# Optimization experiments

Hardware: AMD Instinct MI355X
Metric: run time of the kernel (lower is better)

The kernel has to match this reference:

```python
import jax, jax.numpy as jnp
import numpy as np

D = 768
B = 32
N = 768


def setup_inputs() -> dict:
    key = jax.random.key(0)
    k1, k2, k3, k4 = jax.random.split(key, 4)
    stdv = 1.0 / np.sqrt(D)
    X = jax.random.normal(k1, (B, N, D), dtype=jnp.float32)
    adj = jax.random.uniform(k2, (B, N, N), dtype=jnp.float32)
    W_l = jax.random.uniform(k3, (D, D), dtype=jnp.float32, minval=-stdv, maxval=stdv)
    W_l1 = jax.random.uniform(k4, (D, D), dtype=jnp.float32, minval=-stdv, maxval=stdv)
    return {"X": X, "adj": adj, "W_l": W_l, "W_l1": W_l1}


def _row_normalize(adj):
    # rowsum^-1 with inf -> 0 (rows summing to zero stay zero)
    rowsum = adj.sum(axis=-1, keepdims=True)  # [B, N, 1]
    r_inv = jnp.where(rowsum == 0, 0.0, 1.0 / rowsum)
    return adj * r_inv


def reference(X, adj, W_l, W_l1):
    # X: [B, N, D], adj: [B, N, N]
    adj_n = _row_normalize(adj)
    e1 = jnp.einsum('bnd,de->bne', X, W_l1)        # message transform
    e11 = jnp.einsum('bnm,bmd->bnd', adj_n, e1)    # aggregate
    X1 = jnp.einsum('bnd,de->bne', X, W_l)         # self transform
    h = X1 + e11
    return jax.nn.leaky_relu(h, negative_slope=0.01)
```

## Files before the change

kernel.cpp:

```cpp
#include <hip/hip_runtime.h>
#include <hip/hip_bf16.h>
#include <cstdint>
#include <cstddef>

#define BN_ROWS 24576
#define DD 768
#define BE (768*768)
#define BM 384
#define BN_T 192
#define BK 64

typedef __attribute__((ext_vector_type(8))) short bf16x8;
typedef __attribute__((ext_vector_type(4))) float f32x4;

static __device__ __forceinline__ unsigned short f2bf(float f) {
  unsigned int u = __builtin_bit_cast(unsigned int, f);
  unsigned int lsb = (u >> 16) & 1u;
  u += 0x7fffu + lsb;
  return (unsigned short)(u >> 16);
}


__global__ __launch_bounds__(256) void convertX(const float* __restrict__ x,
                                                unsigned short* __restrict__ xb, int n4) {
  int idx = blockIdx.x * blockDim.x + threadIdx.x;
  int stride = gridDim.x * blockDim.x;
  for (int i = idx; i < n4; i += stride) {
    float4 v = reinterpret_cast<const float4*>(x)[i];
    ushort4 o;
    o.x = f2bf(v.x); o.y = f2bf(v.y); o.z = f2bf(v.z); o.w = f2bf(v.w);
    reinterpret_cast<ushort4*>(xb)[i] = o;
  }
}

__global__ __launch_bounds__(256) void convertWT(const float* __restrict__ Wl,
                                                 const float* __restrict__ Wl1,
                                                 unsigned short* __restrict__ WlT,
                                                 unsigned short* __restrict__ Wl1T) {
  int tid = blockIdx.x * blockDim.x + threadIdx.x;
  if (tid < BE) {
    int d = tid / DD, e = tid % DD;
    WlT[e * DD + d]  = f2bf(Wl[tid]);
    Wl1T[e * DD + d] = f2bf(Wl1[tid]);
  }
}

__global__ __launch_bounds__(256) void adjNorm(const float* __restrict__ adj,
                                               unsigned short* __restrict__ adjnb) {
  int wid = threadIdx.x >> 6, lane = threadIdx.x & 63;
  int row = blockIdx.x * 4 + wid;
  const float4* a = reinterpret_cast<const float4*>(adj + (size_t)row * DD);
  float4 v[3];
  float s = 0.f;
  #pragma unroll
  for (int i = 0; i < 3; ++i) {
    v[i] = a[i * 64 + lane];
    s += (v[i].x + v[i].y) + (v[i].z + v[i].w);
  }
  #pragma unroll
  for (int off = 32; off; off >>= 1) s += __shfl_down(s, off);
  s = __shfl(s, 0);
  float rinv = (s == 0.f) ? 0.f : 1.f / s;
  ushort4* o = reinterpret_cast<ushort4*>(adjnb + (size_t)row * DD);
  #pragma unroll
  for (int i = 0; i < 3; ++i) {
    ushort4 u;
    u.x = f2bf(v[i].x * rinv); u.y = f2bf(v[i].y * rinv);
    u.z = f2bf(v[i].z * rinv); u.w = f2bf(v[i].w * rinv);
    o[i * 64 + lane] = u;
  }
}


template<int MODE>
__global__ __launch_bounds__(512, 2) void gemm8(
    const unsigned short* __restrict__ P0,
    const unsigned short* __restrict__ P1,
    const unsigned short* __restrict__ P2,
    const unsigned short* __restrict__ P3,
    void* __restrict__ outp)
{
  __shared__ char smem[147456];
  constexpr int NT = MODE ? 24 : 12;
  const int tid = threadIdx.x, lane = tid & 63;
  const int wid = tid >> 6, wr = wid >> 1, wc = wid & 1;

  const int logical = (blockIdx.x & 7) * 32 + (blockIdx.x >> 3);

  const unsigned short *Ab0, *Bb0, *Ab1 = nullptr, *Bb1 = nullptr;
  int mt, nt, b;
  if (MODE == 0) {
    mt = logical >> 2; nt = logical & 3;
    b = mt >> 1;
    Ab0 = P0 + (size_t)mt * BM * DD;
    Bb0 = P1 + (size_t)nt * BN_T * DD;
  } else {
    b = logical >> 3; int r = logical & 7; mt = r >> 2; nt = r & 3;
    size_t bo = (size_t)b * BE;
    Ab0 = P0 + bo + (size_t)mt * BM * DD;
    Bb0 = P1 + bo + (size_t)nt * BN_T * DD;
    Ab1 = P2 + bo + (size_t)mt * BM * DD;
    Bb1 = P3 + (size_t)nt * BN_T * DD;
  }

  const int srow = tid >> 3;
  const int sslot = (tid & 7) ^ (srow & 7);
  const int lane_off = srow * DD + sslot * 8;
  const int wchunk = (tid >> 6) * 1024;

  auto stage = [&](int s, int g) {
    int sc = s < NT ? s : 0;
    const unsigned short* base;
    int kk;
    if (MODE == 1 && sc >= 12) { kk = sc - 12; base = (g == 2) ? Bb1 : Ab1; }
    else                       { kk = sc;      base = (g == 2) ? Bb0 : Ab0; }
    const unsigned short* p = base + (size_t)(g == 1 ? 192 : 0) * DD + kk * BK + lane_off;
    char* dst = smem + ((g == 2) ? (98304 + (s & 1) * 24576)
                                 : ((s & 1) * 49152 + g * 24576)) + wchunk;
    #pragma unroll
    for (int i = 0; i < 3; ++i) {
      __builtin_amdgcn_global_load_lds(
          (const __attribute__((address_space(1))) void*)(p + (size_t)i * 64 * DD),
          (__attribute__((address_space(3))) void*)(dst + i * 8192), 16, 0, 0);
    }
  };

  auto frag = [&](int bufbase, int rowbase, int ks) -> bf16x8 {
    int row = rowbase + (lane & 15);
    int slot = (ks * 4 + (lane >> 4)) ^ (row & 7);
    return *reinterpret_cast<const bf16x8*>(smem + bufbase + row * 128 + slot * 16);
  };

  f32x4 acc[6][6] = {};
  bf16x8 af[6], bf[6];

  stage(0, 0); stage(0, 1); stage(0, 2);
  asm volatile("s_waitcnt vmcnt(0)" ::: "memory");
  __builtin_amdgcn_s_barrier();

  for (int t = 0; t < NT; ++t) {
    const int Ab = (t & 1) * 49152;
    const int Bb = 98304 + (t & 1) * 24576;

    #pragma unroll
    for (int i = 0; i < 6; ++i) {
      af[i] = frag(Ab, wr * 96 + i * 16, 0);
      bf[i] = frag(Bb, wc * 96 + i * 16, 0);
    }
    stage(t + 1, 0); stage(t + 1, 1); stage(t + 1, 2);
    __builtin_amdgcn_s_barrier();
    __builtin_amdgcn_s_setprio(1);
    #pragma unroll
    for (int mi = 0; mi < 6; ++mi)
      #pragma unroll
      for (int ni = 0; ni < 6; ++ni)
        acc[mi][ni] = __builtin_amdgcn_mfma_f32_16x16x32_bf16(af[mi], bf[ni], acc[mi][ni], 0, 0, 0);
    __builtin_amdgcn_s_setprio(0);
    __builtin_amdgcn_s_barrier();

    #pragma unroll
    for (int i = 0; i < 6; ++i) {
      af[i] = frag(Ab, wr * 96 + i * 16, 1);
      bf[i] = frag(Bb, wc * 96 + i * 16, 1);
    }
    __builtin_amdgcn_s_barrier();
    __builtin_amdgcn_s_setprio(1);
    #pragma unroll
    for (int mi = 0; mi < 6; ++mi)
      #pragma unroll
      for (int ni = 0; ni < 6; ++ni)
        acc[mi][ni] = __builtin_amdgcn_mfma_f32_16x16x32_bf16(af[mi], bf[ni], acc[mi][ni], 0, 0, 0);
    __builtin_amdgcn_s_setprio(0);
    asm volatile("s_waitcnt vmcnt(0)" ::: "memory");
    __builtin_amdgcn_s_barrier();
  }

  if (MODE == 0) {
    unsigned short* ob = (unsigned short*)outp + (size_t)b * BE;
    const int mloc = (mt & 1) * BM + wr * 96 + (lane >> 4) * 4;
    #pragma unroll
    for (int mi = 0; mi < 6; ++mi)
      #pragma unroll
      for (int ni = 0; ni < 6; ++ni) {
        int m = mloc + mi * 16;
        int d = nt * BN_T + wc * 96 + ni * 16 + (lane & 15);
        f32x4 v = acc[mi][ni];
        ushort4 o;
        o.x = f2bf(v[0]); o.y = f2bf(v[1]); o.z = f2bf(v[2]); o.w = f2bf(v[3]);
        *reinterpret_cast<ushort4*>(ob + (size_t)d * DD + m) = o;
      }
  } else {
    float* ob = (float*)outp + (size_t)b * BE;
    const int mloc = mt * BM + wr * 96 + (lane >> 4) * 4;
    #pragma unroll
    for (int mi = 0; mi < 6; ++mi)
      #pragma unroll
      for (int ni = 0; ni < 6; ++ni) {
        int m = mloc + mi * 16;
        int n = nt * BN_T + wc * 96 + ni * 16 + (lane & 15);
        f32x4 v = acc[mi][ni];
        #pragma unroll
        for (int j = 0; j < 4; ++j) {
          float x = v[j];
          ob[(size_t)(m + j) * DD + n] = x > 0.f ? x : 0.01f * x;
        }
      }
  }
}


extern "C" void kernel_launch(void* const* d_in, const int* in_sizes, int n_in,
                              void* d_out, int out_size, void* d_ws, size_t ws_size,
                              hipStream_t stream) {
  const float* X   = (const float*)d_in[0];
  const float* adj = (const float*)d_in[1];
  const float* Wl  = (const float*)d_in[2];
  const float* Wl1 = (const float*)d_in[3];
  float* out = (float*)d_out;

  char* ws = (char*)d_ws;
  const size_t SZ = (size_t)BN_ROWS * DD * 2;
  unsigned short* Xb    = (unsigned short*)(ws);
  unsigned short* adjnb = (unsigned short*)(ws + SZ);
  unsigned short* e1T   = (unsigned short*)(ws + 2 * SZ);
  unsigned short* WlT   = (unsigned short*)(ws + 3 * SZ);
  unsigned short* Wl1T  = (unsigned short*)(ws + 3 * SZ + (size_t)BE * 2);

  convertX<<<4096, 256, 0, stream>>>(X, Xb, (BN_ROWS * DD) / 4);
  convertWT<<<(BE + 255) / 256, 256, 0, stream>>>(Wl, Wl1, WlT, Wl1T);
  adjNorm<<<BN_ROWS / 4, 256, 0, stream>>>(adj, adjnb);
  gemm8<0><<<256, 512, 0, stream>>>(Xb, Wl1T, nullptr, nullptr, e1T);
  gemm8<1><<<256, 512, 0, stream>>>(adjnb, e1T, Xb, WlT, out);
}
```

Before: 154.5 us.

## Triple-buffer GEMM with BK=32 and tile the weight transpose through LDS

The GEMM main loop moves from a double-buffered BK=64 scheme to a three-stage ring of BK=32 buffers. Loads are issued two stages ahead, partial vmcnt waits replace full drains, and each warp group loads either A or B with a new XOR swizzle. This aims to overlap global-to-LDS traffic with MFMA work and cut LDS use, at the cost of twice as many iterations and barriers. Separately, the weight transpose-convert now goes through a padded shared-memory tile so both reads and writes are coalesced.

```diff
diff --git a/kernel.cpp b/kernel.cpp
--- a/kernel.cpp
+++ b/kernel.cpp
@@ -8,7 +8,9 @@
 #define BE (768*768)
 #define BM 384
 #define BN_T 192
-#define BK 64
+#define BK 32
+#define ABUF 24576
+#define BUFSZ 36864
 
 typedef __attribute__((ext_vector_type(8))) short bf16x8;
 typedef __attribute__((ext_vector_type(4))) float f32x4;
@@ -37,11 +39,27 @@
                                                  const float* __restrict__ Wl1,
                                                  unsigned short* __restrict__ WlT,
                                                  unsigned short* __restrict__ Wl1T) {
-  int tid = blockIdx.x * blockDim.x + threadIdx.x;
-  if (tid < BE) {
-    int d = tid / DD, e = tid % DD;
-    WlT[e * DD + d]  = f2bf(Wl[tid]);
-    Wl1T[e * DD + d] = f2bf(Wl1[tid]);
+  __shared__ float tile[64][65];
+  int tr = blockIdx.x / 12, tc = blockIdx.x % 12;
+  int c = threadIdx.x & 63, r0 = threadIdx.x >> 6;
+  const float* srcs[2] = {Wl, Wl1};
+  unsigned short* dsts[2] = {WlT, Wl1T};
+  #pragma unroll
+  for (int m = 0; m < 2; ++m) {
+    const float* src = srcs[m];
+    #pragma unroll
+    for (int i = 0; i < 16; ++i) {
+      int r = r0 + i * 4;
+      tile[r][c] = src[(size_t)(tr * 64 + r) * DD + tc * 64 + c];
+    }
+    __syncthreads();
+    unsigned short* dst = dsts[m];
+    #pragma unroll
+    for (int i = 0; i < 16; ++i) {
+      int r2 = r0 + i * 4;
+      dst[(size_t)(tc * 64 + r2) * DD + tr * 64 + c] = f2bf(tile[c][r2]);
+    }
+    __syncthreads();
   }
 }
 
@@ -80,8 +98,8 @@
     const unsigned short* __restrict__ P3,
     void* __restrict__ outp)
 {
-  __shared__ char smem[147456];
-  constexpr int NT = MODE ? 24 : 12;
+  __shared__ char smem[3 * BUFSZ];
+  constexpr int NT = MODE ? 48 : 24;
   const int tid = threadIdx.x, lane = tid & 63;
   const int wid = tid >> 6, wr = wid >> 1, wc = wid & 1;
 
@@ -103,75 +121,72 @@
     Bb1 = P3 + (size_t)nt * BN_T * DD;
   }
 
-  const int srow = tid >> 3;
-  const int sslot = (tid & 7) ^ (srow & 7);
-  const int lane_off = srow * DD + sslot * 8;
-  const int wchunk = (tid >> 6) * 1024;
-
-  auto stage = [&](int s, int g) {
+  const int r_in = lane >> 2;
+  const int s_in = lane & 3;
+
+  auto stage = [&](int s) {
     int sc = s < NT ? s : 0;
-    const unsigned short* base;
+    const int buf = (s % 3) * BUFSZ;
+    const unsigned short *Abase, *Bbase;
     int kk;
-    if (MODE == 1 && sc >= 12) { kk = sc - 12; base = (g == 2) ? Bb1 : Ab1; }
-    else                       { kk = sc;      base = (g == 2) ? Bb0 : Ab0; }
-    const unsigned short* p = base + (size_t)(g == 1 ? 192 : 0) * DD + kk * BK + lane_off;
-    char* dst = smem + ((g == 2) ? (98304 + (s & 1) * 24576)
-                                 : ((s & 1) * 49152 + g * 24576)) + wchunk;
-    #pragma unroll
-    for (int i = 0; i < 3; ++i) {
-      __builtin_amdgcn_global_load_lds(
-          (const __attribute__((address_space(1))) void*)(p + (size_t)i * 64 * DD),
-          (__attribute__((address_space(3))) void*)(dst + i * 8192), 16, 0, 0);
+    if (MODE == 1 && sc >= 24) { kk = sc - 24; Abase = Ab1; Bbase = Bb1; }
+    else                       { kk = sc;      Abase = Ab0; Bbase = Bb0; }
+    if (wid < 4) {
+      #pragma unroll
+      for (int i = 0; i < 6; ++i) {
+        int row = wid * 96 + i * 16 + r_in;
+        int slot = s_in ^ ((row >> 1) & 3);
+        const unsigned short* src = Abase + (size_t)row * DD + kk * BK + slot * 8;
+        __builtin_amdgcn_global_load_lds(
+            (const __attribute__((address_space(1))) void*)src,
+            (__attribute__((address_space(3))) void*)(smem + buf + (wid * 96 + i * 16) * 64),
+            16, 0, 0);
+      }
+    } else {
+      #pragma unroll
+      for (int i = 0; i < 3; ++i) {
+        int row = (wid - 4) * 48 + i * 16 + r_in;
+        int slot = s_in ^ ((row >> 1) & 3);
+        const unsigned short* src = Bbase + (size_t)row * DD + kk * BK + slot * 8;
+        __builtin_amdgcn_global_load_lds(
+            (const __attribute__((address_space(1))) void*)src,
+            (__attribute__((address_space(3))) void*)(smem + buf + ABUF + ((wid - 4) * 48 + i * 16) * 64),
+            16, 0, 0);
+      }
     }
   };
 
-  auto frag = [&](int bufbase, int rowbase, int ks) -> bf16x8 {
-    int row = rowbase + (lane & 15);
-    int slot = (ks * 4 + (lane >> 4)) ^ (row & 7);
-    return *reinterpret_cast<const bf16x8*>(smem + bufbase + row * 128 + slot * 16);
+  const int ks = lane >> 4;
+  auto frag = [&](int off, int row) -> bf16x8 {
+    int slot = ks ^ ((row >> 1) & 3);
+    return *reinterpret_cast<const bf16x8*>(smem + off + row * 64 + slot * 16);
   };
 
   f32x4 acc[6][6] = {};
-  bf16x8 af[6], bf[6];
-
-  stage(0, 0); stage(0, 1); stage(0, 2);
-  asm volatile("s_waitcnt vmcnt(0)" ::: "memory");
-  __builtin_amdgcn_s_barrier();
+
+  stage(0); stage(1);
 
   for (int t = 0; t < NT; ++t) {
-    const int Ab = (t & 1) * 49152;
-    const int Bb = 98304 + (t & 1) * 24576;
-
+    stage(t + 2);
+    if (wid < 4) asm volatile("s_waitcnt vmcnt(12)" ::: "memory");
+    else         asm volatile("s_waitcnt vmcnt(6)"  ::: "memory");
+    __builtin_amdgcn_s_barrier();
+
+    const int bufA = (t % 3) * BUFSZ;
+    const int bufB = bufA + ABUF;
+    bf16x8 af[6], bg[6];
     #pragma unroll
     for (int i = 0; i < 6; ++i) {
-      af[i] = frag(Ab, wr * 96 + i * 16, 0);
-      bf[i] = frag(Bb, wc * 96 + i * 16, 0);
-    }
-    stage(t + 1, 0); stage(t + 1, 1); stage(t + 1, 2);
-    __builtin_amdgcn_s_barrier();
+      af[i] = frag(bufA, wr * 96 + i * 16 + (lane & 15));
+      bg[i] = frag(bufB, wc * 96 + i * 16 + (lane & 15));
+    }
     __builtin_amdgcn_s_setprio(1);
     #pragma unroll
     for (int mi = 0; mi < 6; ++mi)
       #pragma unroll
       for (int ni = 0; ni < 6; ++ni)
-        acc[mi][ni] = __builtin_amdgcn_mfma_f32_16x16x32_bf16(af[mi], bf[ni], acc[mi][ni], 0, 0, 0);
+        acc[mi][ni] = __builtin_amdgcn_mfma_f32_16x16x32_bf16(af[mi], bg[ni], acc[mi][ni], 0, 0, 0);
     __builtin_amdgcn_s_setprio(0);
-    __builtin_amdgcn_s_barrier();
-
-    #pragma unroll
-    for (int i = 0; i < 6; ++i) {
-      af[i] = frag(Ab, wr * 96 + i * 16, 1);
-      bf[i] = frag(Bb, wc * 96 + i * 16, 1);
-    }
-    __builtin_amdgcn_s_barrier();
-    __builtin_amdgcn_s_setprio(1);
-    #pragma unroll
-    for (int mi = 0; mi < 6; ++mi)
-      #pragma unroll
-      for (int ni = 0; ni < 6; ++ni)
-        acc[mi][ni] = __builtin_amdgcn_mfma_f32_16x16x32_bf16(af[mi], bf[ni], acc[mi][ni], 0, 0, 0);
-    __builtin_amdgcn_s_setprio(0);
-    asm volatile("s_waitcnt vmcnt(0)" ::: "memory");
     __builtin_amdgcn_s_barrier();
   }
 
@@ -227,7 +242,7 @@
   unsigned short* Wl1T  = (unsigned short*)(ws + 3 * SZ + (size_t)BE * 2);
 
   convertX<<<4096, 256, 0, stream>>>(X, Xb, (BN_ROWS * DD) / 4);
-  convertWT<<<(BE + 255) / 256, 256, 0, stream>>>(Wl, Wl1, WlT, Wl1T);
+  convertWT<<<144, 256, 0, stream>>>(Wl, Wl1, WlT, Wl1T);
   adjNorm<<<BN_ROWS / 4, 256, 0, stream>>>(adj, adjnb);
   gemm8<0><<<256, 512, 0, stream>>>(Xb, Wl1T, nullptr, nullptr, e1T);
   gemm8<1><<<256, 512, 0, stream>>>(adjnb, e1T, Xb, WlT, out);
```

After: 156.0 us. Within noise of the previous version (+1.0%).
